# Kernel tuning notes

Measured on AMD Instinct MI355X. Metric: run time of the kernel, lower is better.

The kernel has to match this reference:

```python
import jax, jax.numpy as jnp
import numpy as np

N_NODES = 100000
N_EDGES = 1600000
IN_FEATS = 256
DIMS = [IN_FEATS, 128, 64, 16, 40]


def setup_inputs() -> dict:
    key = jax.random.key(0)
    ks = jax.random.split(key, 3 + 2 * 4)
    x = jax.random.normal(ks[0], (N_NODES, IN_FEATS), dtype=jnp.float32)
    src = jax.random.randint(ks[1], (N_EDGES,), 0, N_NODES)
    dst = jax.random.randint(ks[2], (N_EDGES,), 0, N_NODES)
    inp = {"x": x, "src": src, "dst": dst}
    for i in range(4):
        fan_in = DIMS[i]
        inp[f"W{i+1}"] = jax.random.normal(ks[3 + 2 * i], (DIMS[i], DIMS[i + 1]), dtype=jnp.float32) / np.sqrt(fan_in)
        inp[f"b{i+1}"] = jnp.zeros((DIMS[i + 1],), dtype=jnp.float32)
    return inp


def reference(x, src, dst, W1, b1, W2, b2, W3, b3, W4, b4):
    n = x.shape[0]
    ones = jnp.ones(src.shape[0], dtype=x.dtype)
    # symmetric GCN normalization (DGL norm='both'); clamp deg>=1 like DGL
    deg_out = jnp.maximum(jax.ops.segment_sum(ones, src, num_segments=n), 1.0)
    deg_in = jnp.maximum(jax.ops.segment_sum(ones, dst, num_segments=n), 1.0)
    norm_src = jax.lax.rsqrt(deg_out)[:, None]  # [N,1]
    norm_dst = jax.lax.rsqrt(deg_in)[:, None]   # [N,1]

    def gconv(h, W, b, act):
        # project first (in_feats >= out_feats for every layer, matching DGL ordering)
        h = (h * norm_src) @ W                                   # [N, d_out]
        h = jax.ops.segment_sum(h[src], dst, num_segments=n)      # SpMM aggregate
        h = h * norm_dst + b
        return jax.nn.relu(h) if act else h

    h = gconv(x, W1, b1, True)
    h = gconv(h, W2, b2, True)
    h = gconv(h, W3, b3, True)
    h = gconv(h, W4, b4, False)
    return h
```

## Files before the change

### kernel.cpp

```cpp
#include <hip/hip_runtime.h>


typedef unsigned short ushort_t;

__device__ __forceinline__ void gload_lds16(const float4* g, float4* l) {
    __builtin_amdgcn_global_load_lds(
        (const __attribute__((address_space(1))) void*)g,
        (__attribute__((address_space(3))) void*)l, 16, 0, 0);
}

__device__ __forceinline__ ushort_t f2bf(float f) {
    unsigned u = __float_as_uint(f);
    u += 0x7FFFu + ((u >> 16) & 1u);
    return (ushort_t)(u >> 16);
}
#define BFLO(u) __uint_as_float((u) << 16)
#define BFHI(u) __uint_as_float((u) & 0xffff0000u)

template<int DIN, int DOUT, int RB, int KT, typename EPI>
__device__ __forceinline__ void proj_body(
        const float* __restrict__ in, const float* __restrict__ W,
        int N, int n0, float4* __restrict__ wlds, float4* __restrict__ xlds,
        EPI&& epi) {
    constexpr int CG  = DOUT / 4;
    constexpr int RPP = 256 / CG;
    constexpr int R4  = RB / RPP;
    constexpr int K4T = KT / 4;
    constexpr int NKT = DIN / KT;
    constexpr int XTILE = RB * K4T;
    constexpr int WTILE = KT * CG;
    static_assert(RPP * CG == 256, "full block");
    static_assert((K4T & (K4T - 1)) == 0, "pow2 swizzle");
    static_assert(XTILE % 256 == 0 && WTILE % 256 == 0, "stage granularity");

    const int tid  = threadIdx.x;
    const int wave = tid >> 6;
    const int lane = tid & 63;
    const int rp   = tid / CG;
    const int cg   = tid - rp * CG;

    float4 acc[R4];
#pragma unroll
    for (int r = 0; r < R4; ++r) acc[r] = make_float4(0.f, 0.f, 0.f, 0.f);

    for (int kt = 0; kt < NKT; ++kt) {
        const float4* wsrc = (const float4*)(W + (size_t)kt * KT * DOUT);
#pragma unroll
        for (int j = 0; j < WTILE / 256; ++j) {
            int base = j * 256 + wave * 64;
            gload_lds16(wsrc + base + lane, &wlds[base]);
        }
#pragma unroll
        for (int j = 0; j < XTILE / 256; ++j) {
            int base = j * 256 + wave * 64;
            int fi   = base + lane;
            int row  = fi / K4T;
            int k4   = fi - row * K4T;
            int k4s  = k4 ^ (row & (K4T - 1));
            int grow = n0 + row; if (grow >= N) grow = N - 1;
            const float4* gsrc = (const float4*)(in + (size_t)grow * DIN) + kt * K4T + k4s;
            gload_lds16(gsrc, &xlds[base]);
        }
        __syncthreads();
#pragma unroll 2
        for (int k4 = 0; k4 < K4T; ++k4) {
            float4 w0 = wlds[(k4 * 4 + 0) * CG + cg];
            float4 w1 = wlds[(k4 * 4 + 1) * CG + cg];
            float4 w2 = wlds[(k4 * 4 + 2) * CG + cg];
            float4 w3 = wlds[(k4 * 4 + 3) * CG + cg];
#pragma unroll
            for (int r = 0; r < R4; ++r) {
                int row = rp + r * RPP;
                float4 xv = xlds[row * K4T + (k4 ^ (row & (K4T - 1)))];
                acc[r].x = fmaf(xv.x, w0.x, acc[r].x);
                acc[r].y = fmaf(xv.x, w0.y, acc[r].y);
                acc[r].z = fmaf(xv.x, w0.z, acc[r].z);
                acc[r].w = fmaf(xv.x, w0.w, acc[r].w);
                acc[r].x = fmaf(xv.y, w1.x, acc[r].x);
                acc[r].y = fmaf(xv.y, w1.y, acc[r].y);
                acc[r].z = fmaf(xv.y, w1.z, acc[r].z);
                acc[r].w = fmaf(xv.y, w1.w, acc[r].w);
                acc[r].x = fmaf(xv.z, w2.x, acc[r].x);
                acc[r].y = fmaf(xv.z, w2.y, acc[r].y);
                acc[r].z = fmaf(xv.z, w2.z, acc[r].z);
                acc[r].w = fmaf(xv.z, w2.w, acc[r].w);
                acc[r].x = fmaf(xv.w, w3.x, acc[r].x);
                acc[r].y = fmaf(xv.w, w3.y, acc[r].y);
                acc[r].z = fmaf(xv.w, w3.z, acc[r].z);
                acc[r].w = fmaf(xv.w, w3.w, acc[r].w);
            }
        }
        __syncthreads();
    }
    epi(acc, rp, cg);
}

template<int DIN, int DOUT, int RB, int KT>
__global__ void __launch_bounds__(256) k_comb(
        const float* __restrict__ x, const float* __restrict__ W,
        ushort_t* __restrict__ outbf, int N,
        const int* __restrict__ src, const int* __restrict__ dst,
        int* __restrict__ degO, int* __restrict__ degI,
        int* __restrict__ rank, int E, int PB, int HTH) {
    constexpr int CG  = DOUT / 4;
    constexpr int RPP = 256 / CG;
    constexpr int R4  = RB / RPP;
    constexpr int K4T = KT / 4;
    __shared__ float4 wlds[KT * CG];
    __shared__ float4 xlds[RB * K4T];

    int bid = blockIdx.x, g = bid / 5, r = bid - g * 5;
    if (r >= 3) {
        int i = (g * 2 + (r - 3)) * 256 + (int)threadIdx.x;
        for (; i < E; i += HTH) {
            atomicAdd(&degO[src[i]], 1);
            rank[i] = atomicAdd(&degI[dst[i]], 1);
        }
        return;
    }
    int pidx = g * 3 + r;
    if (pidx >= PB) return;
    int n0 = pidx * RB;
    proj_body<DIN, DOUT, RB, KT>(x, W, N, n0, wlds, xlds,
        [&](float4 (&acc)[R4], int rp, int cg) {
#pragma unroll
            for (int rr = 0; rr < R4; ++rr) {
                int n = n0 + rp + rr * RPP;
                if (n < N) {
                    ushort4 s;
                    s.x = f2bf(acc[rr].x); s.y = f2bf(acc[rr].y);
                    s.z = f2bf(acc[rr].z); s.w = f2bf(acc[rr].w);
                    *(ushort4*)(outbf + (size_t)n * DOUT + cg * 4) = s;
                }
            }
        });
}

template<int DIN, int DOUT, int RB, int KT>
__global__ void __launch_bounds__(256) k_proj_gl2b(
        const float* __restrict__ in, const float* __restrict__ nrm,
        const float* __restrict__ W, ushort_t* __restrict__ outbf, int N) {
    constexpr int CG  = DOUT / 4;
    constexpr int RPP = 256 / CG;
    constexpr int R4  = RB / RPP;
    constexpr int K4T = KT / 4;
    __shared__ float4 wlds[KT * CG];
    __shared__ float4 xlds[RB * K4T];
    int n0 = blockIdx.x * RB;
    proj_body<DIN, DOUT, RB, KT>(in, W, N, n0, wlds, xlds,
        [&](float4 (&acc)[R4], int rp, int cg) {
#pragma unroll
            for (int rr = 0; rr < R4; ++rr) {
                int n = n0 + rp + rr * RPP;
                if (n < N) {
                    float nm = nrm[n];
                    ushort4 s;
                    s.x = f2bf(acc[rr].x * nm); s.y = f2bf(acc[rr].y * nm);
                    s.z = f2bf(acc[rr].z * nm); s.w = f2bf(acc[rr].w * nm);
                    *(ushort4*)(outbf + (size_t)n * DOUT + cg * 4) = s;
                }
            }
        });
}

template<int DIN, int DOUT, int R4, int KT, int EPI>
__global__ void __launch_bounds__(256) k_proj_lds(
        const float* __restrict__ in, const float* __restrict__ nrm,
        const float* __restrict__ W, const float* __restrict__ bias,
        float* __restrict__ out, int N) {
    constexpr int CG  = DOUT / 4;
    constexpr int RPP = 256 / CG;
    constexpr int RB  = RPP * R4;
    constexpr int NKT = DIN / KT;
    __shared__ float4 wlds[KT * CG];

    int tid = threadIdx.x;
    int rp  = tid / CG;
    int cg  = tid - rp * CG;
    bool active = (rp < RPP);
    int n0 = blockIdx.x * RB;

    int nrow[R4];
    const float4* xr[R4];
#pragma unroll
    for (int r = 0; r < R4; ++r) {
        int n = n0 + rp + r * RPP;
        nrow[r] = n;
        int nc = n < N ? n : N - 1;
        xr[r] = (const float4*)(in + (size_t)nc * DIN);
    }
    float4 acc[R4];
#pragma unroll
    for (int r = 0; r < R4; ++r) acc[r] = make_float4(0.f, 0.f, 0.f, 0.f);

    for (int kt = 0; kt < NKT; ++kt) {
        const float4* wsrc = (const float4*)(W + (size_t)kt * KT * DOUT);
        for (int i = tid; i < KT * CG; i += 256) wlds[i] = wsrc[i];
        __syncthreads();
        if (active) {
#pragma unroll 2
            for (int k4 = 0; k4 < KT / 4; ++k4) {
                float4 w0 = wlds[(k4 * 4 + 0) * CG + cg];
                float4 w1 = wlds[(k4 * 4 + 1) * CG + cg];
                float4 w2 = wlds[(k4 * 4 + 2) * CG + cg];
                float4 w3 = wlds[(k4 * 4 + 3) * CG + cg];
#pragma unroll
                for (int r = 0; r < R4; ++r) {
                    float4 xv = xr[r][kt * (KT / 4) + k4];
                    acc[r].x = fmaf(xv.x, w0.x, acc[r].x);
                    acc[r].y = fmaf(xv.x, w0.y, acc[r].y);
                    acc[r].z = fmaf(xv.x, w0.z, acc[r].z);
                    acc[r].w = fmaf(xv.x, w0.w, acc[r].w);
                    acc[r].x = fmaf(xv.y, w1.x, acc[r].x);
                    acc[r].y = fmaf(xv.y, w1.y, acc[r].y);
                    acc[r].z = fmaf(xv.y, w1.z, acc[r].z);
                    acc[r].w = fmaf(xv.y, w1.w, acc[r].w);
                    acc[r].x = fmaf(xv.z, w2.x, acc[r].x);
                    acc[r].y = fmaf(xv.z, w2.y, acc[r].y);
                    acc[r].z = fmaf(xv.z, w2.z, acc[r].z);
                    acc[r].w = fmaf(xv.z, w2.w, acc[r].w);
                    acc[r].x = fmaf(xv.w, w3.x, acc[r].x);
                    acc[r].y = fmaf(xv.w, w3.y, acc[r].y);
                    acc[r].z = fmaf(xv.w, w3.z, acc[r].z);
                    acc[r].w = fmaf(xv.w, w3.w, acc[r].w);
                }
            }
        }
        __syncthreads();
    }
    if (active) {
#pragma unroll
        for (int r = 0; r < R4; ++r) {
            int n = nrow[r];
            if (n < N) {
                float nm = nrm[n];
                float4 o;
                if (EPI == 0) {
                    o = make_float4(acc[r].x * nm, acc[r].y * nm,
                                    acc[r].z * nm, acc[r].w * nm);
                } else {
                    float4 b = *(const float4*)(bias + cg * 4);
                    o.x = fmaf(acc[r].x, nm, b.x);
                    o.y = fmaf(acc[r].y, nm, b.y);
                    o.z = fmaf(acc[r].z, nm, b.z);
                    o.w = fmaf(acc[r].w, nm, b.w);
                }
                *(float4*)(out + (size_t)n * DOUT + cg * 4) = o;
            }
        }
    }
}

__global__ void k_blocksum(const int* __restrict__ degI, const int* __restrict__ degO,
                           int* __restrict__ bsum, float* __restrict__ nSf,
                           float* __restrict__ nDf, int N) {
    __shared__ int sh[256];
    int base = blockIdx.x * 1024;
    int s = 0;
    for (int i = threadIdx.x; i < 1024; i += 256) {
        int idx = base + i;
        if (idx < N) {
            int d = degI[idx];
            s += d;
            nDf[idx] = rsqrtf((float)(d > 1 ? d : 1));
            int a = degO[idx];
            nSf[idx] = rsqrtf((float)(a > 1 ? a : 1));
        }
    }
    sh[threadIdx.x] = s; __syncthreads();
    for (int off = 128; off > 0; off >>= 1) {
        if (threadIdx.x < off) sh[threadIdx.x] += sh[threadIdx.x + off];
        __syncthreads();
    }
    if (threadIdx.x == 0) bsum[blockIdx.x] = sh[0];
}

__global__ void k_scan_bsums(const int* __restrict__ bsum, int* __restrict__ boffs, int nb) {
    if (blockIdx.x == 0 && threadIdx.x == 0) {
        int run = 0;
        for (int i = 0; i < nb; ++i) { boffs[i] = run; run += bsum[i]; }
    }
}

__global__ void k_blockscan(const int* __restrict__ deg, const int* __restrict__ boffs,
                            int* __restrict__ rowptr, int N) {
    __shared__ int sh[256];
    int base = blockIdx.x * 1024;
    int i0 = base + threadIdx.x * 4;
    int v[4]; int tot = 0;
#pragma unroll
    for (int r = 0; r < 4; ++r) {
        int idx = i0 + r;
        v[r] = (idx < N) ? deg[idx] : 0;
        tot += v[r];
    }
    sh[threadIdx.x] = tot; __syncthreads();
    for (int off = 1; off < 256; off <<= 1) {
        int t = (threadIdx.x >= off) ? sh[threadIdx.x - off] : 0;
        __syncthreads();
        sh[threadIdx.x] += t;
        __syncthreads();
    }
    int run = sh[threadIdx.x] - tot + boffs[blockIdx.x];
#pragma unroll
    for (int r = 0; r < 4; ++r) {
        int idx = i0 + r;
        if (idx < N) rowptr[idx] = run;
        run += v[r];
    }
}

__global__ void k_fill3(const int* __restrict__ src, const int* __restrict__ dst,
                        const int* __restrict__ rank, const int* __restrict__ rowptr,
                        int* __restrict__ col, int E) {
    int stride = gridDim.x * blockDim.x;
    for (int i = blockIdx.x * blockDim.x + threadIdx.x; i < E; i += stride) {
        col[rowptr[dst[i]] + rank[i]] = src[i];
    }
}

template<int DOUT, bool EDGESCALE>
__global__ void __launch_bounds__(256) k_gather_b(
        const int* __restrict__ rowptr, const int* __restrict__ col,
        const int* __restrict__ degI, const float* __restrict__ nSf,
        const float* __restrict__ nDf, const ushort_t* __restrict__ projbf,
        const float* __restrict__ bias, float* __restrict__ out, int N) {
    constexpr int CGB = DOUT / 8;
    long t = blockIdx.x * 256L + threadIdx.x;
    if (t >= (long)N * CGB) return;
    int n  = (int)(t / CGB);
    int cb = (int)(t - (long)n * CGB);
    int beg = rowptr[n];
    int dg  = degI[n];
    float acc[8];
#pragma unroll
    for (int k = 0; k < 8; ++k) acc[k] = 0.f;
    int i = 0;
    for (; i + 2 <= dg; i += 2) {
        int s0 = col[beg + i];
        int s1 = col[beg + i + 1];
        uint4 v0 = *(const uint4*)(projbf + (size_t)s0 * DOUT + cb * 8);
        uint4 v1 = *(const uint4*)(projbf + (size_t)s1 * DOUT + cb * 8);
        float ns0 = EDGESCALE ? nSf[s0] : 1.f;
        float ns1 = EDGESCALE ? nSf[s1] : 1.f;
        if (EDGESCALE) {
            acc[0] = fmaf(ns0, BFLO(v0.x), acc[0]);
            acc[1] = fmaf(ns0, BFHI(v0.x), acc[1]);
            acc[2] = fmaf(ns0, BFLO(v0.y), acc[2]);
            acc[3] = fmaf(ns0, BFHI(v0.y), acc[3]);
            acc[4] = fmaf(ns0, BFLO(v0.z), acc[4]);
            acc[5] = fmaf(ns0, BFHI(v0.z), acc[5]);
            acc[6] = fmaf(ns0, BFLO(v0.w), acc[6]);
            acc[7] = fmaf(ns0, BFHI(v0.w), acc[7]);
            acc[0] = fmaf(ns1, BFLO(v1.x), acc[0]);
            acc[1] = fmaf(ns1, BFHI(v1.x), acc[1]);
            acc[2] = fmaf(ns1, BFLO(v1.y), acc[2]);
            acc[3] = fmaf(ns1, BFHI(v1.y), acc[3]);
            acc[4] = fmaf(ns1, BFLO(v1.z), acc[4]);
            acc[5] = fmaf(ns1, BFHI(v1.z), acc[5]);
            acc[6] = fmaf(ns1, BFLO(v1.w), acc[6]);
            acc[7] = fmaf(ns1, BFHI(v1.w), acc[7]);
        } else {
            acc[0] += BFLO(v0.x) + BFLO(v1.x);
            acc[1] += BFHI(v0.x) + BFHI(v1.x);
            acc[2] += BFLO(v0.y) + BFLO(v1.y);
            acc[3] += BFHI(v0.y) + BFHI(v1.y);
            acc[4] += BFLO(v0.z) + BFLO(v1.z);
            acc[5] += BFHI(v0.z) + BFHI(v1.z);
            acc[6] += BFLO(v0.w) + BFLO(v1.w);
            acc[7] += BFHI(v0.w) + BFHI(v1.w);
        }
    }
    if (i < dg) {
        int s0 = col[beg + i];
        uint4 v0 = *(const uint4*)(projbf + (size_t)s0 * DOUT + cb * 8);
        float ns0 = EDGESCALE ? nSf[s0] : 1.f;
        acc[0] = fmaf(ns0, BFLO(v0.x), acc[0]);
        acc[1] = fmaf(ns0, BFHI(v0.x), acc[1]);
        acc[2] = fmaf(ns0, BFLO(v0.y), acc[2]);
        acc[3] = fmaf(ns0, BFHI(v0.y), acc[3]);
        acc[4] = fmaf(ns0, BFLO(v0.z), acc[4]);
        acc[5] = fmaf(ns0, BFHI(v0.z), acc[5]);
        acc[6] = fmaf(ns0, BFLO(v0.w), acc[6]);
        acc[7] = fmaf(ns0, BFHI(v0.w), acc[7]);
    }
    float nm = nDf[n];
    const float* bp = bias + cb * 8;
    float o[8];
#pragma unroll
    for (int k = 0; k < 8; ++k) o[k] = fmaxf(fmaf(acc[k], nm, bp[k]), 0.f);
    float* dstp = out + (size_t)n * DOUT + cb * 8;
    *(float4*)(dstp)     = make_float4(o[0], o[1], o[2], o[3]);
    *(float4*)(dstp + 4) = make_float4(o[4], o[5], o[6], o[7]);
}

template<int DOUT, bool RELU, bool NORMBIAS, bool SCALESRC>
__global__ void __launch_bounds__(256) k_gather(
        const int* __restrict__ rowptr, const int* __restrict__ col,
        const int* __restrict__ degI, const float* __restrict__ nSf,
        const float* __restrict__ nDf, const float* __restrict__ proj,
        const float* __restrict__ bias, float* __restrict__ out, int N) {
    constexpr int CG = DOUT / 4;
    long t = blockIdx.x * 256L + threadIdx.x;
    if (t >= (long)N * CG) return;
    int n  = (int)(t / CG);
    int cg = (int)(t - (long)n * CG);
    int beg = rowptr[n];
    int dg  = degI[n];
    float4 a0 = make_float4(0.f, 0.f, 0.f, 0.f);
    float4 a1 = make_float4(0.f, 0.f, 0.f, 0.f);
    float4 a2 = make_float4(0.f, 0.f, 0.f, 0.f);
    float4 a3 = make_float4(0.f, 0.f, 0.f, 0.f);
    int i = 0;
    for (; i + 4 <= dg; i += 4) {
        int s0 = col[beg + i];
        int s1 = col[beg + i + 1];
        int s2 = col[beg + i + 2];
        int s3 = col[beg + i + 3];
        float4 v0 = *(const float4*)(proj + (size_t)s0 * DOUT + cg * 4);
        float4 v1 = *(const float4*)(proj + (size_t)s1 * DOUT + cg * 4);
        float4 v2 = *(const float4*)(proj + (size_t)s2 * DOUT + cg * 4);
        float4 v3 = *(const float4*)(proj + (size_t)s3 * DOUT + cg * 4);
        a0.x += v0.x; a0.y += v0.y; a0.z += v0.z; a0.w += v0.w;
        a1.x += v1.x; a1.y += v1.y; a1.z += v1.z; a1.w += v1.w;
        a2.x += v2.x; a2.y += v2.y; a2.z += v2.z; a2.w += v2.w;
        a3.x += v3.x; a3.y += v3.y; a3.z += v3.z; a3.w += v3.w;
    }
    for (; i < dg; ++i) {
        int s0 = col[beg + i];
        float4 v0 = *(const float4*)(proj + (size_t)s0 * DOUT + cg * 4);
        a0.x += v0.x; a0.y += v0.y; a0.z += v0.z; a0.w += v0.w;
    }
    float4 o = make_float4(a0.x + a1.x + a2.x + a3.x,
                           a0.y + a1.y + a2.y + a3.y,
                           a0.z + a1.z + a2.z + a3.z,
                           a0.w + a1.w + a2.w + a3.w);
    if (NORMBIAS) {
        float nm = nDf[n];
        float4 b = *(const float4*)(bias + cg * 4);
        o.x = fmaf(o.x, nm, b.x);
        o.y = fmaf(o.y, nm, b.y);
        o.z = fmaf(o.z, nm, b.z);
        o.w = fmaf(o.w, nm, b.w);
    }
    if (RELU) {
        o.x = fmaxf(o.x, 0.f); o.y = fmaxf(o.y, 0.f);
        o.z = fmaxf(o.z, 0.f); o.w = fmaxf(o.w, 0.f);
    }
    if (SCALESRC) {
        float ns = nSf[n];
        o.x *= ns; o.y *= ns; o.z *= ns; o.w *= ns;
    }
    *(float4*)(out + (size_t)n * DOUT + cg * 4) = o;
}

static inline int cdiv(long a, int b) { return (int)((a + b - 1) / b); }

extern "C" void kernel_launch(void* const* d_in, const int* in_sizes, int n_in,
                              void* d_out, int out_size, void* d_ws, size_t ws_size,
                              hipStream_t stream) {
    const float* x   = (const float*)d_in[0];
    const int*   src = (const int*)d_in[1];
    const int*   dst = (const int*)d_in[2];
    const float* W1 = (const float*)d_in[3];  const float* b1 = (const float*)d_in[4];
    const float* W2 = (const float*)d_in[5];  const float* b2 = (const float*)d_in[6];
    const float* W3 = (const float*)d_in[7];  const float* b3 = (const float*)d_in[8];
    const float* W4 = (const float*)d_in[9];  const float* b4 = (const float*)d_in[10];

    const int N = in_sizes[0] / 256;
    const int E = in_sizes[1];

    int* ws_i = (int*)d_ws;
    int* degO   = ws_i;
    int* degI   = ws_i + N;
    int* rowptr = ws_i + 2 * (size_t)N;
    int* col    = ws_i + 3 * (size_t)N;
    int* rank   = ws_i + 3 * (size_t)N + E;
    float* nSf  = (float*)(ws_i + 3 * (size_t)N + 2 * (size_t)E);
    float* nDf  = nSf + N;
    float* projb = nDf + N;
    float* hbuf  = projb + (size_t)N * 64;
    ushort_t* projbf = (ushort_t*)projb;
    int* bsum   = (int*)hbuf;
    int* boffs  = bsum + 4096;

    int nb = (N + 1023) / 1024;
    int PB = cdiv(N, 64);
    int G5 = cdiv(PB, 3);
    int HTH = (2 * G5) * 256;

    hipMemsetAsync(degO, 0, 2 * (size_t)N * sizeof(int), stream);
    k_comb<256, 128, 64, 32><<<5 * G5, 256, 0, stream>>>(
        x, W1, projbf, N, src, dst, degO, degI, rank, E, PB, HTH);

    k_blocksum<<<nb, 256, 0, stream>>>(degI, degO, bsum, nSf, nDf, N);
    k_scan_bsums<<<1, 64, 0, stream>>>(bsum, boffs, nb);
    k_blockscan<<<nb, 256, 0, stream>>>(degI, boffs, rowptr, N);
    k_fill3<<<2048, 256, 0, stream>>>(src, dst, rank, rowptr, col, E);

    k_gather_b<128, true><<<cdiv((long)N * 16, 256), 256, 0, stream>>>(
        rowptr, col, degI, nSf, nDf, projbf, b1, hbuf, N);

    k_proj_gl2b<128, 64, 64, 32><<<cdiv(N, 64), 256, 0, stream>>>(
        hbuf, nSf, W2, projbf, N);
    k_gather_b<64, false><<<cdiv((long)N * 8, 256), 256, 0, stream>>>(
        rowptr, col, degI, nSf, nDf, projbf, b2, hbuf, N);

    k_proj_lds<64, 16, 1, 64, 0><<<cdiv(N, 64), 256, 0, stream>>>(
        hbuf, nSf, W3, nullptr, projb, N);
    k_gather<16, true, true, true><<<cdiv((long)N * 4, 256), 256, 0, stream>>>(
        rowptr, col, degI, nSf, nDf, projb, b3, hbuf, N);

    k_gather<16, false, false, false><<<cdiv((long)N * 4, 256), 256, 0, stream>>>(
        rowptr, col, degI, nSf, nDf, hbuf, nullptr, projb, N);
    k_proj_lds<16, 40, 2, 16, 1><<<cdiv(N, 50), 256, 0, stream>>>(
        projb, nDf, W4, b4, (float*)d_out, N);
}
```

Baseline: 385.2 us.

## Fuse layer-3 and layer-4 projections into gather epilogues; rebalance degree-count blocks

Layer 2's gather now applies bias, ReLU and source scaling, then multiplies by W3 using wavefront shuffles, so the separate layer-3 projection kernel and its intermediate round trip go away. The layer-4 gather likewise applies W4 and the bias in its epilogue instead of launching a separate projection. The combined degree/projection kernel now gives one of every five blocks to the degree atomics instead of two. The first-layer gather unrolls to four edges per iteration. Fewer launches and less intermediate traffic come at the cost of extra shuffle and LDS work in the gathers, and fewer threads issuing the degree atomics.

```diff
diff --git a/kernel.cpp b/kernel.cpp
--- a/kernel.cpp
+++ b/kernel.cpp
@@ -110,15 +110,15 @@
     __shared__ float4 xlds[RB * K4T];
 
     int bid = blockIdx.x, g = bid / 5, r = bid - g * 5;
-    if (r >= 3) {
-        int i = (g * 2 + (r - 3)) * 256 + (int)threadIdx.x;
+    if (r == 4) {
+        int i = g * 256 + (int)threadIdx.x;
         for (; i < E; i += HTH) {
             atomicAdd(&degO[src[i]], 1);
             rank[i] = atomicAdd(&degI[dst[i]], 1);
         }
         return;
     }
-    int pidx = g * 3 + r;
+    int pidx = g * 4 + r;
     if (pidx >= PB) return;
     int n0 = pidx * RB;
     proj_body<DIN, DOUT, RB, KT>(x, W, N, n0, wlds, xlds,
@@ -161,94 +161,6 @@
                 }
             }
         });
-}
-
-template<int DIN, int DOUT, int R4, int KT, int EPI>
-__global__ void __launch_bounds__(256) k_proj_lds(
-        const float* __restrict__ in, const float* __restrict__ nrm,
-        const float* __restrict__ W, const float* __restrict__ bias,
-        float* __restrict__ out, int N) {
-    constexpr int CG  = DOUT / 4;
-    constexpr int RPP = 256 / CG;
-    constexpr int RB  = RPP * R4;
-    constexpr int NKT = DIN / KT;
-    __shared__ float4 wlds[KT * CG];
-
-    int tid = threadIdx.x;
-    int rp  = tid / CG;
-    int cg  = tid - rp * CG;
-    bool active = (rp < RPP);
-    int n0 = blockIdx.x * RB;
-
-    int nrow[R4];
-    const float4* xr[R4];
-#pragma unroll
-    for (int r = 0; r < R4; ++r) {
-        int n = n0 + rp + r * RPP;
-        nrow[r] = n;
-        int nc = n < N ? n : N - 1;
-        xr[r] = (const float4*)(in + (size_t)nc * DIN);
-    }
-    float4 acc[R4];
-#pragma unroll
-    for (int r = 0; r < R4; ++r) acc[r] = make_float4(0.f, 0.f, 0.f, 0.f);
-
-    for (int kt = 0; kt < NKT; ++kt) {
-        const float4* wsrc = (const float4*)(W + (size_t)kt * KT * DOUT);
-        for (int i = tid; i < KT * CG; i += 256) wlds[i] = wsrc[i];
-        __syncthreads();
-        if (active) {
-#pragma unroll 2
-            for (int k4 = 0; k4 < KT / 4; ++k4) {
-                float4 w0 = wlds[(k4 * 4 + 0) * CG + cg];
-                float4 w1 = wlds[(k4 * 4 + 1) * CG + cg];
-                float4 w2 = wlds[(k4 * 4 + 2) * CG + cg];
-                float4 w3 = wlds[(k4 * 4 + 3) * CG + cg];
-#pragma unroll
-                for (int r = 0; r < R4; ++r) {
-                    float4 xv = xr[r][kt * (KT / 4) + k4];
-                    acc[r].x = fmaf(xv.x, w0.x, acc[r].x);
-                    acc[r].y = fmaf(xv.x, w0.y, acc[r].y);
-                    acc[r].z = fmaf(xv.x, w0.z, acc[r].z);
-                    acc[r].w = fmaf(xv.x, w0.w, acc[r].w);
-                    acc[r].x = fmaf(xv.y, w1.x, acc[r].x);
-                    acc[r].y = fmaf(xv.y, w1.y, acc[r].y);
-                    acc[r].z = fmaf(xv.y, w1.z, acc[r].z);
-                    acc[r].w = fmaf(xv.y, w1.w, acc[r].w);
-                    acc[r].x = fmaf(xv.z, w2.x, acc[r].x);
-                    acc[r].y = fmaf(xv.z, w2.y, acc[r].y);
-                    acc[r].z = fmaf(xv.z, w2.z, acc[r].z);
-                    acc[r].w = fmaf(xv.z, w2.w, acc[r].w);
-                    acc[r].x = fmaf(xv.w, w3.x, acc[r].x);
-                    acc[r].y = fmaf(xv.w, w3.y, acc[r].y);
-                    acc[r].z = fmaf(xv.w, w3.z, acc[r].z);
-                    acc[r].w = fmaf(xv.w, w3.w, acc[r].w);
-                }
-            }
-        }
-        __syncthreads();
-    }
-    if (active) {
-#pragma unroll
-        for (int r = 0; r < R4; ++r) {
-            int n = nrow[r];
-            if (n < N) {
-                float nm = nrm[n];
-                float4 o;
-                if (EPI == 0) {
-                    o = make_float4(acc[r].x * nm, acc[r].y * nm,
-                                    acc[r].z * nm, acc[r].w * nm);
-                } else {
-                    float4 b = *(const float4*)(bias + cg * 4);
-                    o.x = fmaf(acc[r].x, nm, b.x);
-                    o.y = fmaf(acc[r].y, nm, b.y);
-                    o.z = fmaf(acc[r].z, nm, b.z);
-                    o.w = fmaf(acc[r].w, nm, b.w);
-                }
-                *(float4*)(out + (size_t)n * DOUT + cg * 4) = o;
-            }
-        }
-    }
 }
 
 __global__ void k_blocksum(const int* __restrict__ degI, const int* __restrict__ degO,
@@ -319,12 +231,12 @@
     }
 }
 
-template<int DOUT, bool EDGESCALE>
-__global__ void __launch_bounds__(256) k_gather_b(
+__global__ void __launch_bounds__(256) k_gather_l1(
         const int* __restrict__ rowptr, const int* __restrict__ col,
         const int* __restrict__ degI, const float* __restrict__ nSf,
         const float* __restrict__ nDf, const ushort_t* __restrict__ projbf,
         const float* __restrict__ bias, float* __restrict__ out, int N) {
+    constexpr int DOUT = 128;
     constexpr int CGB = DOUT / 8;
     long t = blockIdx.x * 256L + threadIdx.x;
     if (t >= (long)N * CGB) return;
@@ -336,45 +248,27 @@
 #pragma unroll
     for (int k = 0; k < 8; ++k) acc[k] = 0.f;
     int i = 0;
-    for (; i + 2 <= dg; i += 2) {
-        int s0 = col[beg + i];
-        int s1 = col[beg + i + 1];
+    for (; i + 4 <= dg; i += 4) {
+        int s0 = col[beg + i],     s1 = col[beg + i + 1];
+        int s2 = col[beg + i + 2], s3 = col[beg + i + 3];
         uint4 v0 = *(const uint4*)(projbf + (size_t)s0 * DOUT + cb * 8);
         uint4 v1 = *(const uint4*)(projbf + (size_t)s1 * DOUT + cb * 8);
-        float ns0 = EDGESCALE ? nSf[s0] : 1.f;
-        float ns1 = EDGESCALE ? nSf[s1] : 1.f;
-        if (EDGESCALE) {
-            acc[0] = fmaf(ns0, BFLO(v0.x), acc[0]);
-            acc[1] = fmaf(ns0, BFHI(v0.x), acc[1]);
-            acc[2] = fmaf(ns0, BFLO(v0.y), acc[2]);
-            acc[3] = fmaf(ns0, BFHI(v0.y), acc[3]);
-            acc[4] = fmaf(ns0, BFLO(v0.z), acc[4]);
-            acc[5] = fmaf(ns0, BFHI(v0.z), acc[5]);
-            acc[6] = fmaf(ns0, BFLO(v0.w), acc[6]);
-            acc[7] = fmaf(ns0, BFHI(v0.w), acc[7]);
-            acc[0] = fmaf(ns1, BFLO(v1.x), acc[0]);
-            acc[1] = fmaf(ns1, BFHI(v1.x), acc[1]);
-            acc[2] = fmaf(ns1, BFLO(v1.y), acc[2]);
-            acc[3] = fmaf(ns1, BFHI(v1.y), acc[3]);
-            acc[4] = fmaf(ns1, BFLO(v1.z), acc[4]);
-            acc[5] = fmaf(ns1, BFHI(v1.z), acc[5]);
-            acc[6] = fmaf(ns1, BFLO(v1.w), acc[6]);
-            acc[7] = fmaf(ns1, BFHI(v1.w), acc[7]);
-        } else {
-            acc[0] += BFLO(v0.x) + BFLO(v1.x);
-            acc[1] += BFHI(v0.x) + BFHI(v1.x);
-            acc[2] += BFLO(v0.y) + BFLO(v1.y);
-            acc[3] += BFHI(v0.y) + BFHI(v1.y);
-            acc[4] += BFLO(v0.z) + BFLO(v1.z);
-            acc[5] += BFHI(v0.z) + BFHI(v1.z);
-            acc[6] += BFLO(v0.w) + BFLO(v1.w);
-            acc[7] += BFHI(v0.w) + BFHI(v1.w);
-        }
-    }
-    if (i < dg) {
+        uint4 v2 = *(const uint4*)(projbf + (size_t)s2 * DOUT + cb * 8);
+        uint4 v3 = *(const uint4*)(projbf + (size_t)s3 * DOUT + cb * 8);
+        float n0 = nSf[s0], n1 = nSf[s1], n2 = nSf[s2], n3 = nSf[s3];
+        acc[0] = fmaf(n0, BFLO(v0.x), fmaf(n1, BFLO(v1.x), fmaf(n2, BFLO(v2.x), fmaf(n3, BFLO(v3.x), acc[0]))));
+        acc[1] = fmaf(n0, BFHI(v0.x), fmaf(n1, BFHI(v1.x), fmaf(n2, BFHI(v2.x), fmaf(n3, BFHI(v3.x), acc[1]))));
+        acc[2] = fmaf(n0, BFLO(v0.y), fmaf(n1, BFLO(v1.y), fmaf(n2, BFLO(v2.y), fmaf(n3, BFLO(v3.y), acc[2]))));
+        acc[3] = fmaf(n0, BFHI(v0.y), fmaf(n1, BFHI(v1.y), fmaf(n2, BFHI(v2.y), fmaf(n3, BFHI(v3.y), acc[3]))));
+        acc[4] = fmaf(n0, BFLO(v0.z), fmaf(n1, BFLO(v1.z), fmaf(n2, BFLO(v2.z), fmaf(n3, BFLO(v3.z), acc[4]))));
+        acc[5] = fmaf(n0, BFHI(v0.z), fmaf(n1, BFHI(v1.z), fmaf(n2, BFHI(v2.z), fmaf(n3, BFHI(v3.z), acc[5]))));
+        acc[6] = fmaf(n0, BFLO(v0.w), fmaf(n1, BFLO(v1.w), fmaf(n2, BFLO(v2.w), fmaf(n3, BFLO(v3.w), acc[6]))));
+        acc[7] = fmaf(n0, BFHI(v0.w), fmaf(n1, BFHI(v1.w), fmaf(n2, BFHI(v2.w), fmaf(n3, BFHI(v3.w), acc[7]))));
+    }
+    for (; i < dg; ++i) {
         int s0 = col[beg + i];
         uint4 v0 = *(const uint4*)(projbf + (size_t)s0 * DOUT + cb * 8);
-        float ns0 = EDGESCALE ? nSf[s0] : 1.f;
+        float ns0 = nSf[s0];
         acc[0] = fmaf(ns0, BFLO(v0.x), acc[0]);
         acc[1] = fmaf(ns0, BFHI(v0.x), acc[1]);
         acc[2] = fmaf(ns0, BFLO(v0.y), acc[2]);
@@ -394,17 +288,81 @@
     *(float4*)(dstp + 4) = make_float4(o[4], o[5], o[6], o[7]);
 }
 
-template<int DOUT, bool RELU, bool NORMBIAS, bool SCALESRC>
-__global__ void __launch_bounds__(256) k_gather(
+__global__ void __launch_bounds__(256) k_gather_fuse2(
+        const int* __restrict__ rowptr, const int* __restrict__ col,
+        const int* __restrict__ degI, const float* __restrict__ nSf,
+        const float* __restrict__ nDf, const ushort_t* __restrict__ p2bf,
+        const float* __restrict__ b2, const float* __restrict__ W3,
+        float* __restrict__ P3, int N) {
+    constexpr int DOUT = 64;
+    __shared__ float w3s[64 * 16];
+    ((float4*)w3s)[threadIdx.x] = ((const float4*)W3)[threadIdx.x];
+    __syncthreads();
+
+    long t = blockIdx.x * 256L + threadIdx.x;
+    int n = (int)(t >> 3);
+    bool valid = n < N;
+    if (!valid) n = N - 1;
+    int cb = (int)(t & 7);
+    int lane = threadIdx.x & 63;
+    int gb = lane & ~7;
+
+    int beg = rowptr[n];
+    int dg  = degI[n];
+    float acc[8];
+#pragma unroll
+    for (int k = 0; k < 8; ++k) acc[k] = 0.f;
+    int i = 0;
+    for (; i + 4 <= dg; i += 4) {
+        int s0 = col[beg + i],     s1 = col[beg + i + 1];
+        int s2 = col[beg + i + 2], s3 = col[beg + i + 3];
+        uint4 v0 = *(const uint4*)(p2bf + (size_t)s0 * DOUT + cb * 8);
+        uint4 v1 = *(const uint4*)(p2bf + (size_t)s1 * DOUT + cb * 8);
+        uint4 v2 = *(const uint4*)(p2bf + (size_t)s2 * DOUT + cb * 8);
+        uint4 v3 = *(const uint4*)(p2bf + (size_t)s3 * DOUT + cb * 8);
+        acc[0] += BFLO(v0.x) + BFLO(v1.x) + BFLO(v2.x) + BFLO(v3.x);
+        acc[1] += BFHI(v0.x) + BFHI(v1.x) + BFHI(v2.x) + BFHI(v3.x);
+        acc[2] += BFLO(v0.y) + BFLO(v1.y) + BFLO(v2.y) + BFLO(v3.y);
+        acc[3] += BFHI(v0.y) + BFHI(v1.y) + BFHI(v2.y) + BFHI(v3.y);
+        acc[4] += BFLO(v0.z) + BFLO(v1.z) + BFLO(v2.z) + BFLO(v3.z);
+        acc[5] += BFHI(v0.z) + BFHI(v1.z) + BFHI(v2.z) + BFHI(v3.z);
+        acc[6] += BFLO(v0.w) + BFLO(v1.w) + BFLO(v2.w) + BFLO(v3.w);
+        acc[7] += BFHI(v0.w) + BFHI(v1.w) + BFHI(v2.w) + BFHI(v3.w);
+    }
+    for (; i < dg; ++i) {
+        int s0 = col[beg + i];
+        uint4 v0 = *(const uint4*)(p2bf + (size_t)s0 * DOUT + cb * 8);
+        acc[0] += BFLO(v0.x); acc[1] += BFHI(v0.x);
+        acc[2] += BFLO(v0.y); acc[3] += BFHI(v0.y);
+        acc[4] += BFLO(v0.z); acc[5] += BFHI(v0.z);
+        acc[6] += BFLO(v0.w); acc[7] += BFHI(v0.w);
+    }
+    float nm = nDf[n];
+    float ns = nSf[n];
+    const float* bp = b2 + cb * 8;
+    float o[8];
+#pragma unroll
+    for (int k = 0; k < 8; ++k)
+        o[k] = fmaxf(fmaf(acc[k], nm, bp[k]), 0.f) * ns;
+    float y0 = 0.f, y1 = 0.f;
+#pragma unroll
+    for (int k = 0; k < 64; ++k) {
+        float v = __shfl(o[k & 7], gb + (k >> 3), 64);
+        y0 = fmaf(v, w3s[k * 16 + 2 * cb], y0);
+        y1 = fmaf(v, w3s[k * 16 + 2 * cb + 1], y1);
+    }
+    if (valid) *(float2*)(P3 + (size_t)n * 16 + 2 * cb) = make_float2(y0, y1);
+}
+
+__global__ void __launch_bounds__(256) k_gather_l3(
         const int* __restrict__ rowptr, const int* __restrict__ col,
         const int* __restrict__ degI, const float* __restrict__ nSf,
         const float* __restrict__ nDf, const float* __restrict__ proj,
         const float* __restrict__ bias, float* __restrict__ out, int N) {
-    constexpr int CG = DOUT / 4;
     long t = blockIdx.x * 256L + threadIdx.x;
-    if (t >= (long)N * CG) return;
-    int n  = (int)(t / CG);
-    int cg = (int)(t - (long)n * CG);
+    if (t >= (long)N * 4) return;
+    int n  = (int)(t >> 2);
+    int cg = (int)(t & 3);
     int beg = rowptr[n];
     int dg  = degI[n];
     float4 a0 = make_float4(0.f, 0.f, 0.f, 0.f);
@@ -413,14 +371,12 @@
     float4 a3 = make_float4(0.f, 0.f, 0.f, 0.f);
     int i = 0;
     for (; i + 4 <= dg; i += 4) {
-        int s0 = col[beg + i];
-        int s1 = col[beg + i + 1];
-        int s2 = col[beg + i + 2];
-        int s3 = col[beg + i + 3];
-        float4 v0 = *(const float4*)(proj + (size_t)s0 * DOUT + cg * 4);
-        float4 v1 = *(const float4*)(proj + (size_t)s1 * DOUT + cg * 4);
-        float4 v2 = *(const float4*)(proj + (size_t)s2 * DOUT + cg * 4);
-        float4 v3 = *(const float4*)(proj + (size_t)s3 * DOUT + cg * 4);
+        int s0 = col[beg + i],     s1 = col[beg + i + 1];
+        int s2 = col[beg + i + 2], s3 = col[beg + i + 3];
+        float4 v0 = *(const float4*)(proj + (size_t)s0 * 16 + cg * 4);
+        float4 v1 = *(const float4*)(proj + (size_t)s1 * 16 + cg * 4);
+        float4 v2 = *(const float4*)(proj + (size_t)s2 * 16 + cg * 4);
+        float4 v3 = *(const float4*)(proj + (size_t)s3 * 16 + cg * 4);
         a0.x += v0.x; a0.y += v0.y; a0.z += v0.z; a0.w += v0.w;
         a1.x += v1.x; a1.y += v1.y; a1.z += v1.z; a1.w += v1.w;
         a2.x += v2.x; a2.y += v2.y; a2.z += v2.z; a2.w += v2.w;
@@ -428,30 +384,78 @@
     }
     for (; i < dg; ++i) {
         int s0 = col[beg + i];
-        float4 v0 = *(const float4*)(proj + (size_t)s0 * DOUT + cg * 4);
+        float4 v0 = *(const float4*)(proj + (size_t)s0 * 16 + cg * 4);
         a0.x += v0.x; a0.y += v0.y; a0.z += v0.z; a0.w += v0.w;
     }
-    float4 o = make_float4(a0.x + a1.x + a2.x + a3.x,
-                           a0.y + a1.y + a2.y + a3.y,
-                           a0.z + a1.z + a2.z + a3.z,
-                           a0.w + a1.w + a2.w + a3.w);
-    if (NORMBIAS) {
+    float4 s = make_float4(a0.x + a1.x + a2.x + a3.x, a0.y + a1.y + a2.y + a3.y,
+                           a0.z + a1.z + a2.z + a3.z, a0.w + a1.w + a2.w + a3.w);
+    float nm = nDf[n];
+    float ns = nSf[n];
+    float4 b = *(const float4*)(bias + cg * 4);
+    float4 o;
+    o.x = fmaxf(fmaf(s.x, nm, b.x), 0.f) * ns;
+    o.y = fmaxf(fmaf(s.y, nm, b.y), 0.f) * ns;
+    o.z = fmaxf(fmaf(s.z, nm, b.z), 0.f) * ns;
+    o.w = fmaxf(fmaf(s.w, nm, b.w), 0.f) * ns;
+    *(float4*)(out + (size_t)n * 16 + cg * 4) = o;
+}
+
+__global__ void __launch_bounds__(256) k_gather_fuse4(
+        const int* __restrict__ rowptr, const int* __restrict__ col,
+        const int* __restrict__ degI, const float* __restrict__ nDf,
+        const float* __restrict__ t4, const float* __restrict__ W4,
+        const float* __restrict__ b4, float* __restrict__ out, int N) {
+    __shared__ float w4s[16 * 40];
+    __shared__ float b4s[40];
+    for (int i = threadIdx.x; i < 160; i += 256)
+        ((float4*)w4s)[i] = ((const float4*)W4)[i];
+    if (threadIdx.x < 40) b4s[threadIdx.x] = b4[threadIdx.x];
+    __syncthreads();
+
+    long t = blockIdx.x * 256L + threadIdx.x;
+    int n = (int)(t >> 2);
+    bool valid = n < N;
+    if (!valid) n = N - 1;
+    int cg = (int)(t & 3);
+    int lane = threadIdx.x & 63;
+    int gb = lane & ~3;
+
+    int beg = rowptr[n];
+    int dg  = degI[n];
+    float4 a0 = make_float4(0.f, 0.f, 0.f, 0.f);
+    float4 a1 = make_float4(0.f, 0.f, 0.f, 0.f);
+    int i = 0;
+    for (; i + 2 <= dg; i += 2) {
+        int s0 = col[beg + i], s1 = col[beg + i + 1];
+        float4 v0 = *(const float4*)(t4 + (size_t)s0 * 16 + cg * 4);
+        float4 v1 = *(const float4*)(t4 + (size_t)s1 * 16 + cg * 4);
+        a0.x += v0.x; a0.y += v0.y; a0.z += v0.z; a0.w += v0.w;
+        a1.x += v1.x; a1.y += v1.y; a1.z += v1.z; a1.w += v1.w;
+    }
+    if (i < dg) {
+        int s0 = col[beg + i];
+        float4 v0 = *(const float4*)(t4 + (size_t)s0 * 16 + cg * 4);
+        a0.x += v0.x; a0.y += v0.y; a0.z += v0.z; a0.w += v0.w;
+    }
+    float av[4] = { a0.x + a1.x, a0.y + a1.y, a0.z + a1.z, a0.w + a1.w };
+
+    float y[10];
+#pragma unroll
+    for (int jj = 0; jj < 10; ++jj) y[jj] = 0.f;
+#pragma unroll
+    for (int k = 0; k < 16; ++k) {
+        float v = __shfl(av[k & 3], gb + (k >> 2), 64);
+        const float* wr = w4s + k * 40 + cg * 10;
+#pragma unroll
+        for (int jj = 0; jj < 10; ++jj) y[jj] = fmaf(v, wr[jj], y[jj]);
+    }
+    if (valid) {
         float nm = nDf[n];
-        float4 b = *(const float4*)(bias + cg * 4);
-        o.x = fmaf(o.x, nm, b.x);
-        o.y = fmaf(o.y, nm, b.y);
-        o.z = fmaf(o.z, nm, b.z);
-        o.w = fmaf(o.w, nm, b.w);
-    }
-    if (RELU) {
-        o.x = fmaxf(o.x, 0.f); o.y = fmaxf(o.y, 0.f);
-        o.z = fmaxf(o.z, 0.f); o.w = fmaxf(o.w, 0.f);
-    }
-    if (SCALESRC) {
-        float ns = nSf[n];
-        o.x *= ns; o.y *= ns; o.z *= ns; o.w *= ns;
-    }
-    *(float4*)(out + (size_t)n * DOUT + cg * 4) = o;
+        float* dp = out + (size_t)n * 40 + cg * 10;
+        const float* bp = b4s + cg * 10;
+#pragma unroll
+        for (int jj = 0; jj < 10; ++jj) dp[jj] = fmaf(y[jj], nm, bp[jj]);
+    }
 }
 
 static inline int cdiv(long a, int b) { return (int)((a + b - 1) / b); }
@@ -481,13 +485,14 @@
     float* projb = nDf + N;
     float* hbuf  = projb + (size_t)N * 64;
     ushort_t* projbf = (ushort_t*)projb;
+    float* P3 = projb + (size_t)N * 32;
     int* bsum   = (int*)hbuf;
     int* boffs  = bsum + 4096;
 
     int nb = (N + 1023) / 1024;
     int PB = cdiv(N, 64);
-    int G5 = cdiv(PB, 3);
-    int HTH = (2 * G5) * 256;
+    int G5 = cdiv(PB, 4);
+    int HTH = G5 * 256;
 
     hipMemsetAsync(degO, 0, 2 * (size_t)N * sizeof(int), stream);
     k_comb<256, 128, 64, 32><<<5 * G5, 256, 0, stream>>>(
@@ -498,21 +503,17 @@
     k_blockscan<<<nb, 256, 0, stream>>>(degI, boffs, rowptr, N);
     k_fill3<<<2048, 256, 0, stream>>>(src, dst, rank, rowptr, col, E);
 
-    k_gather_b<128, true><<<cdiv((long)N * 16, 256), 256, 0, stream>>>(
+    k_gather_l1<<<cdiv((long)N * 16, 256), 256, 0, stream>>>(
         rowptr, col, degI, nSf, nDf, projbf, b1, hbuf, N);
 
     k_proj_gl2b<128, 64, 64, 32><<<cdiv(N, 64), 256, 0, stream>>>(
         hbuf, nSf, W2, projbf, N);
-    k_gather_b<64, false><<<cdiv((long)N * 8, 256), 256, 0, stream>>>(
-        rowptr, col, degI, nSf, nDf, projbf, b2, hbuf, N);
-
-    k_proj_lds<64, 16, 1, 64, 0><<<cdiv(N, 64), 256, 0, stream>>>(
-        hbuf, nSf, W3, nullptr, projb, N);
-    k_gather<16, true, true, true><<<cdiv((long)N * 4, 256), 256, 0, stream>>>(
-        rowptr, col, degI, nSf, nDf, projb, b3, hbuf, N);
-
-    k_gather<16, false, false, false><<<cdiv((long)N * 4, 256), 256, 0, stream>>>(
-        rowptr, col, degI, nSf, nDf, hbuf, nullptr, projb, N);
-    k_proj_lds<16, 40, 2, 16, 1><<<cdiv(N, 50), 256, 0, stream>>>(
-        projb, nDf, W4, b4, (float*)d_out, N);
-}
+    k_gather_fuse2<<<cdiv((long)N * 8, 256), 256, 0, stream>>>(
+        rowptr, col, degI, nSf, nDf, projbf, b2, W3, P3, N);
+
+    k_gather_l3<<<cdiv((long)N * 4, 256), 256, 0, stream>>>(
+        rowptr, col, degI, nSf, nDf, P3, b3, hbuf, N);
+
+    k_gather_fuse4<<<cdiv((long)N * 4, 256), 256, 0, stream>>>(
+        rowptr, col, degI, nDf, hbuf, W4, b4, (float*)d_out, N);
+}
```

Result: no change. 377.9 us (-1.9%).
